# Kernel optimization log

Measured on AMD Instinct MI355X. Metric: run time of the kernel, lower is better.

Reference implementation:

```python
import jax, jax.numpy as jnp
import numpy as np

ALPHA = 0.2          # LeakyReLU negative slope
NEG_INF = -9e15      # masking value from the original module


def setup_inputs() -> dict:
    key = jax.random.key(0)
    kw, ka, k1, k2, k3 = jax.random.split(key, 5)
    B, N1, N2, F, O = 4, 2048, 2048, 256, 256
    word = jax.random.normal(kw, (B, N2, F), dtype=jnp.float32)
    # 0/1 hypergraph incidence matrix (float, as in the torch module)
    adj = jax.random.randint(ka, (B, N1, N2), 0, 2).astype(jnp.float32)
    stdv = 1.0 / np.sqrt(O)
    W1 = jax.random.uniform(k1, (F, O), jnp.float32, -stdv, stdv)
    W2 = jax.random.uniform(k2, (F, O), jnp.float32, -stdv, stdv)
    w3 = jax.random.uniform(k3, (2 * O, 1), jnp.float32, -stdv, stdv)
    return {"word": word, "adj": adj, "W1": W1, "W2": W2, "w3": w3}


def reference(word, adj, W1, W2, w3):
    # word: [B, N2, F]; adj: [B, N1, N2]; W1/W2: [F, O]; w3: [2O, 1]
    O = W1.shape[1]
    # mean-pool neighbor features per hyperedge (row-normalized adj)
    deg = jnp.sum(adj, axis=-1, keepdims=True)                 # [B, N1, 1]
    deg = jnp.where(deg > 0, deg, jnp.ones_like(deg))
    mp = jnp.matmul(adj / deg, word)                           # [B, N1, F]
    # The original builds 4D tensors h1[b,i,j,:] = adj[b,i,j]*word[b,j,:] and
    # h_mp[b,i,j,:] = adj[b,i,j]*mp[b,i,:], projects both and dots with w3.
    # Since scaling commutes with the linear maps, the scalar score is
    #   adj[b,i,j] * (word[b,j] @ W1 @ w3_a + mp[b,i] @ W2 @ w3_b)
    w3a = w3[:O, 0]                                            # pairs with w1h
    w3b = w3[O:, 0]                                            # pairs with w2h
    s1 = jnp.einsum('bnf,fo,o->bn', word, W1, w3a)             # [B, N2]
    s2 = jnp.einsum('bnf,fo,o->bn', mp, W2, w3b)               # [B, N1]
    pre = adj * (s2[:, :, None] + s1[:, None, :])              # [B, N1, N2]
    alpha = jnp.exp(jax.nn.leaky_relu(pre, ALPHA))
    attention = jnp.where(adj > 0, alpha, NEG_INF)
    attention_edge = jax.nn.softmax(attention, axis=2)         # over N2
    edge = jnp.matmul(attention_edge, word)                    # [B, N1, F]
    return edge
```

## Files before the change

kernel.cpp:

```cpp
#include <hip/hip_runtime.h>

#define B 4
#define N 2048
#define F 256
#define O 256
#define LOG2E 1.4426950408889634f
#define NEG_BIG -9000000000000000.0f

typedef _Float16 f16;
typedef f16 f16x4 __attribute__((ext_vector_type(4)));
typedef f16 f16x8 __attribute__((ext_vector_type(8)));
typedef float f32x4 __attribute__((ext_vector_type(4)));

#define WS_V1 0
#define WS_V2 256
#define WS_T1 512
#define WS_T2 (512 + B*N)
#define WT_OFF (1u << 20)
#define MK_OFF (6u << 20)

__device__ __forceinline__ float alpha_of(float pre2) {
  return __builtin_amdgcn_exp2f(fmaxf(pre2, 0.2f * pre2));
}

__global__ __launch_bounds__(256) void k_mask(const float* __restrict__ adj,
                                              unsigned* __restrict__ maskg) {
  int t = threadIdx.x;
  int wv = t >> 6, l = t & 63;
  int row = blockIdx.x * 4 + wv;
  const float* arow = adj + (size_t)row * N;
  unsigned mb = 0u;
  #pragma unroll
  for (int i = 0; i < 8; ++i) {
    float4 av = *(const float4*)(arow + i * 256 + l * 4);
    mb |= (av.x > 0.f ? (1u << (4 * i + 0)) : 0u) |
          (av.y > 0.f ? (1u << (4 * i + 1)) : 0u) |
          (av.z > 0.f ? (1u << (4 * i + 2)) : 0u) |
          (av.w > 0.f ? (1u << (4 * i + 3)) : 0u);
  }
  maskg[(size_t)row * 64 + l] = mb;
}

__global__ __launch_bounds__(256) void k_v(const float* __restrict__ W1,
                                           const float* __restrict__ W2,
                                           const float* __restrict__ w3,
                                           float* __restrict__ ws) {
  int tid = threadIdx.x;
  int lane = tid & 63;
  int f = blockIdx.x * 4 + (tid >> 6);
  float a = 0.f, b = 0.f;
  #pragma unroll
  for (int k = 0; k < 4; ++k) {
    int o = lane + 64 * k;
    a += W1[f * O + o] * w3[o];
    b += W2[f * O + o] * w3[O + o];
  }
  #pragma unroll
  for (int off = 32; off > 0; off >>= 1) {
    a += __shfl_down(a, off);
    b += __shfl_down(b, off);
  }
  if (lane == 0) {
    ws[WS_V1 + f] = a;
    ws[WS_V2 + f] = b;
  }
}

__global__ __launch_bounds__(256) void k_prep(const float* __restrict__ word,
                                              float* __restrict__ ws,
                                              f16* __restrict__ wordT) {
  __shared__ float v1s[F], v2s[F];
  __shared__ __align__(16) f16 tile[F][40];
  int t = threadIdx.x;
  int k0 = blockIdx.x * 32;
  int b = blockIdx.y;

  if (t < 64)       ((float4*)v1s)[t]      = ((const float4*)(ws + WS_V1))[t];
  else if (t < 128) ((float4*)v2s)[t - 64] = ((const float4*)(ws + WS_V2))[t - 64];
  __syncthreads();

  int r = t >> 3;
  int cg = t & 7;
  const float* wrow = word + ((size_t)(b * N + k0 + r)) * F;
  float a = 0.f, bb = 0.f;
  #pragma unroll
  for (int i = 0; i < 8; ++i) {
    int c = i * 32 + cg * 4;
    float4 w = *(const float4*)(wrow + c);
    float4 x1 = *(const float4*)(v1s + c);
    float4 x2 = *(const float4*)(v2s + c);
    a  += w.x * x1.x + w.y * x1.y + w.z * x1.z + w.w * x1.w;
    bb += w.x * x2.x + w.y * x2.y + w.z * x2.z + w.w * x2.w;
    tile[c + 0][r] = (f16)w.x;
    tile[c + 1][r] = (f16)w.y;
    tile[c + 2][r] = (f16)w.z;
    tile[c + 3][r] = (f16)w.w;
  }
  #pragma unroll
  for (int off = 4; off > 0; off >>= 1) {
    a  += __shfl_down(a, off);
    bb += __shfl_down(bb, off);
  }
  if (cg == 0) {
    ws[WS_T1 + b * N + k0 + r] = a * LOG2E;
    ws[WS_T2 + b * N + k0 + r] = bb;
  }
  __syncthreads();

  size_t base = (size_t)b * F * N;
  int kc = k0 >> 5;
  #pragma unroll
  for (int s = 0; s < 4; ++s) {
    int u = t + 256 * s;
    int ft = u >> 6, l2 = u & 63;
    f16x8 h = *(const f16x8*)&tile[ft * 16 + (l2 & 15)][(l2 >> 4) * 8];
    *(f16x8*)(wordT + base + ((size_t)(ft * 64 + kc) * 64 + l2) * 8) = h;
  }
}

__global__ __launch_bounds__(1024, 4) void k_sg(const unsigned* __restrict__ maskg,
                                                const float* __restrict__ ws,
                                                const f16* __restrict__ wordT,
                                                float* __restrict__ out) {
  extern __shared__ __align__(16) char smem[];
  float* t1S = (float*)(smem + 131072);
  float* t2S = (float*)(smem + 139264);

  const int t = threadIdx.x;
  const int wv = t >> 6, l = t & 63;
  const int bid = blockIdx.x;
  const int sbid = (bid & 7) * 32 + (bid >> 3);
  const int row0 = sbid * 32;
  const int b = row0 >> 11;

  if (t < 512) {
    *(float4*)(t1S + t * 4) = *(const float4*)(ws + WS_T1 + b * N + t * 4);
  } else {
    int u = t - 512;
    *(float4*)(t2S + u * 4) = *(const float4*)(ws + WS_T2 + b * N + u * 4);
  }
  __syncthreads();

  #pragma unroll 1
  for (int rr = 0; rr < 2; ++rr) {
    const int lrow = wv * 2 + rr;
    const unsigned mb = maskg[(size_t)(row0 + lrow) * 64 + l];

    float deg = (float)__builtin_popcount(mb);
    float dot = 0.f;
    #pragma unroll
    for (int i = 0; i < 8; ++i) {
      float4 uv = *(const float4*)(t2S + i * 256 + l * 4);
      dot += (((mb >> (4 * i + 0)) & 1u) ? uv.x : 0.f);
      dot += (((mb >> (4 * i + 1)) & 1u) ? uv.y : 0.f);
      dot += (((mb >> (4 * i + 2)) & 1u) ? uv.z : 0.f);
      dot += (((mb >> (4 * i + 3)) & 1u) ? uv.w : 0.f);
    }
    #pragma unroll
    for (int off = 32; off > 0; off >>= 1) {
      deg += __shfl_xor(deg, off);
      dot += __shfl_xor(dot, off);
    }
    float degc = deg > 0.f ? deg : 1.f;
    float s2p = (dot / degc) * LOG2E;

    float al[32];
    float m = NEG_BIG;
    #pragma unroll
    for (int i = 0; i < 8; ++i) {
      float4 pv = *(const float4*)(t1S + i * 256 + l * 4);
      const float p[4] = {pv.x, pv.y, pv.z, pv.w};
      #pragma unroll
      for (int c = 0; c < 4; ++c) {
        int j = 4 * i + c;
        al[j] = ((mb >> j) & 1u) ? alpha_of(p[c] + s2p) : NEG_BIG;
        m = fmaxf(m, al[j]);
      }
    }
    #pragma unroll
    for (int off = 32; off > 0; off >>= 1) m = fmaxf(m, __shfl_xor(m, off));

    float negmL = -m * LOG2E;
    float z = 0.f;
    #pragma unroll
    for (int j = 0; j < 32; ++j) {
      float e = __builtin_amdgcn_exp2f(fmaf(al[j], LOG2E, negmL));
      z += e;
      al[j] = e;
    }
    #pragma unroll
    for (int off = 32; off > 0; off >>= 1) z += __shfl_xor(z, off);
    float sc, wn;
    if (deg > 0.f) { sc = 1.0f / z; wn = 0.f; }
    else           { sc = 0.f;      wn = 1.0f / (float)N; }

    #pragma unroll
    for (int i = 0; i < 8; ++i) {
      f16x4 h;
      #pragma unroll
      for (int c = 0; c < 4; ++c) {
        int j = 4 * i + c;
        float w = ((mb >> j) & 1u) ? al[j] * sc : wn;
        h[c] = (f16)w;
      }
      unsigned byteoff = (unsigned)(lrow * 4096 + i * 512 + l * 8) ^ ((unsigned)(lrow & 7) << 4);
      *(f16x4*)(smem + byteoff) = h;
    }
  }
  __syncthreads();

  const int ftile = wv;
  const unsigned abase = (unsigned)((l & 15) * 4096 + (l >> 4) * 16);
  const unsigned ax = ((unsigned)(l & 7)) << 4;
  const f16* bp = wordT + (size_t)b * (F * N) + ((size_t)ftile * 64 * 64 + (size_t)l) * 8;

  f32x4 acc0 = {0.f, 0.f, 0.f, 0.f};
  f32x4 acc1 = {0.f, 0.f, 0.f, 0.f};
  #pragma unroll 8
  for (int kc = 0; kc < 64; ++kc) {
    f16x8 bf = *(const f16x8*)(bp + (size_t)kc * 512);
    f16x8 a0 = *(const f16x8*)(smem + ((abase + kc * 64) ^ ax));
    f16x8 a1 = *(const f16x8*)(smem + ((abase + 16 * 4096 + kc * 64) ^ ax));
    acc0 = __builtin_amdgcn_mfma_f32_16x16x32_f16(a0, bf, acc0, 0, 0, 0);
    acc1 = __builtin_amdgcn_mfma_f32_16x16x32_f16(a1, bf, acc1, 0, 0, 0);
  }

  const int orow = row0 + (l >> 4) * 4;
  const int c0 = ftile * 16 + (l & 15);
  #pragma unroll
  for (int reg = 0; reg < 4; ++reg) {
    out[(size_t)(orow + reg) * F + c0]      = acc0[reg];
    out[(size_t)(orow + 16 + reg) * F + c0] = acc1[reg];
  }
}

extern "C" void kernel_launch(void* const* d_in, const int* in_sizes, int n_in,
                              void* d_out, int out_size, void* d_ws, size_t ws_size,
                              hipStream_t stream) {
  const float* word = (const float*)d_in[0];
  const float* adj  = (const float*)d_in[1];
  const float* W1   = (const float*)d_in[2];
  const float* W2   = (const float*)d_in[3];
  const float* w3   = (const float*)d_in[4];
  float* out = (float*)d_out;
  float* ws  = (float*)d_ws;
  f16* wordT = (f16*)((char*)d_ws + WT_OFF);
  unsigned* maskg = (unsigned*)((char*)d_ws + MK_OFF);

  static bool s_attr = false;
  if (!s_attr) {
    hipFuncSetAttribute((const void*)k_sg, hipFuncAttributeMaxDynamicSharedMemorySize, 147456);
    s_attr = true;
  }

  k_mask<<<(B * N) / 4, 256, 0, stream>>>(adj, maskg);
  k_v<<<64, 256, 0, stream>>>(W1, W2, w3, ws);
  k_prep<<<dim3(N / 32, B), 256, 0, stream>>>(word, ws, wordT);
  k_sg<<<(B * N) / 32, 1024, 147456, stream>>>(maskg, ws, wordT, out);
}
```

Measured before the change: 130.5 us.

## Merge mask, projection-vector and prep kernels into one launch

Folds the adjacency-bitmask kernel, the W·w3 vector kernel and the word-prep kernel into a single launch. The first 2048 blocks build the mask and the remaining 256 each recompute the projection vectors redundantly before transposing word tiles. This removes two kernel launches and their serialization, and lets mask building overlap with prep work. The cost is each prep block re-reading all of W1/W2. The main kernel also hoists its mask loads ahead of the shared-memory staging barrier.

```diff
diff --git a/kernel.cpp b/kernel.cpp
--- a/kernel.cpp
+++ b/kernel.cpp
@@ -12,8 +12,6 @@
 typedef f16 f16x8 __attribute__((ext_vector_type(8)));
 typedef float f32x4 __attribute__((ext_vector_type(4)));
 
-#define WS_V1 0
-#define WS_V2 256
 #define WS_T1 512
 #define WS_T2 (512 + B*N)
 #define WT_OFF (1u << 20)
@@ -23,60 +21,60 @@
   return __builtin_amdgcn_exp2f(fmaxf(pre2, 0.2f * pre2));
 }
 
-__global__ __launch_bounds__(256) void k_mask(const float* __restrict__ adj,
-                                              unsigned* __restrict__ maskg) {
-  int t = threadIdx.x;
-  int wv = t >> 6, l = t & 63;
-  int row = blockIdx.x * 4 + wv;
-  const float* arow = adj + (size_t)row * N;
-  unsigned mb = 0u;
-  #pragma unroll
-  for (int i = 0; i < 8; ++i) {
-    float4 av = *(const float4*)(arow + i * 256 + l * 4);
-    mb |= (av.x > 0.f ? (1u << (4 * i + 0)) : 0u) |
-          (av.y > 0.f ? (1u << (4 * i + 1)) : 0u) |
-          (av.z > 0.f ? (1u << (4 * i + 2)) : 0u) |
-          (av.w > 0.f ? (1u << (4 * i + 3)) : 0u);
-  }
-  maskg[(size_t)row * 64 + l] = mb;
-}
-
-__global__ __launch_bounds__(256) void k_v(const float* __restrict__ W1,
-                                           const float* __restrict__ W2,
-                                           const float* __restrict__ w3,
-                                           float* __restrict__ ws) {
-  int tid = threadIdx.x;
-  int lane = tid & 63;
-  int f = blockIdx.x * 4 + (tid >> 6);
-  float a = 0.f, b = 0.f;
-  #pragma unroll
-  for (int k = 0; k < 4; ++k) {
-    int o = lane + 64 * k;
-    a += W1[f * O + o] * w3[o];
-    b += W2[f * O + o] * w3[O + o];
-  }
-  #pragma unroll
-  for (int off = 32; off > 0; off >>= 1) {
-    a += __shfl_down(a, off);
-    b += __shfl_down(b, off);
-  }
-  if (lane == 0) {
-    ws[WS_V1 + f] = a;
-    ws[WS_V2 + f] = b;
-  }
-}
-
-__global__ __launch_bounds__(256) void k_prep(const float* __restrict__ word,
-                                              float* __restrict__ ws,
-                                              f16* __restrict__ wordT) {
+__global__ __launch_bounds__(256) void k_mp(const float* __restrict__ adj,
+                                            const float* __restrict__ word,
+                                            const float* __restrict__ W1,
+                                            const float* __restrict__ W2,
+                                            const float* __restrict__ w3,
+                                            float* __restrict__ ws,
+                                            f16* __restrict__ wordT,
+                                            unsigned* __restrict__ maskg) {
+  __shared__ float w3s[2 * O];
   __shared__ float v1s[F], v2s[F];
   __shared__ __align__(16) f16 tile[F][40];
-  int t = threadIdx.x;
-  int k0 = blockIdx.x * 32;
-  int b = blockIdx.y;
-
-  if (t < 64)       ((float4*)v1s)[t]      = ((const float4*)(ws + WS_V1))[t];
-  else if (t < 128) ((float4*)v2s)[t - 64] = ((const float4*)(ws + WS_V2))[t - 64];
+  const int bid = blockIdx.x;
+  const int t = threadIdx.x;
+
+  if (bid < 2048) {
+    int wv = t >> 6, l = t & 63;
+    int row = bid * 4 + wv;
+    const float* arow = adj + (size_t)row * N;
+    unsigned mb = 0u;
+    #pragma unroll
+    for (int i = 0; i < 8; ++i) {
+      float4 av = *(const float4*)(arow + i * 256 + l * 4);
+      mb |= (av.x > 0.f ? (1u << (4 * i + 0)) : 0u) |
+            (av.y > 0.f ? (1u << (4 * i + 1)) : 0u) |
+            (av.z > 0.f ? (1u << (4 * i + 2)) : 0u) |
+            (av.w > 0.f ? (1u << (4 * i + 3)) : 0u);
+    }
+    maskg[(size_t)row * 64 + l] = mb;
+    return;
+  }
+
+  const int p = bid - 2048;
+  const int k0 = (p & 63) * 32;
+  const int b = p >> 6;
+
+  if (t < 128) ((float4*)w3s)[t] = ((const float4*)w3)[t];
+  __syncthreads();
+
+  {
+    float va = 0.f, vb = 0.f;
+    const float* r1 = W1 + (size_t)t * O;
+    const float* r2 = W2 + (size_t)t * O;
+    #pragma unroll 8
+    for (int i = 0; i < 64; ++i) {
+      float4 x1 = *(const float4*)(r1 + i * 4);
+      float4 x2 = *(const float4*)(r2 + i * 4);
+      va += x1.x * w3s[i * 4] + x1.y * w3s[i * 4 + 1] +
+            x1.z * w3s[i * 4 + 2] + x1.w * w3s[i * 4 + 3];
+      vb += x2.x * w3s[O + i * 4] + x2.y * w3s[O + i * 4 + 1] +
+            x2.z * w3s[O + i * 4 + 2] + x2.w * w3s[O + i * 4 + 3];
+    }
+    v1s[t] = va;
+    v2s[t] = vb;
+  }
   __syncthreads();
 
   int r = t >> 3;
@@ -133,6 +131,9 @@
   const int row0 = sbid * 32;
   const int b = row0 >> 11;
 
+  const unsigned mb0 = maskg[(size_t)(row0 + wv * 2) * 64 + l];
+  const unsigned mb1 = maskg[(size_t)(row0 + wv * 2 + 1) * 64 + l];
+
   if (t < 512) {
     *(float4*)(t1S + t * 4) = *(const float4*)(ws + WS_T1 + b * N + t * 4);
   } else {
@@ -144,7 +145,7 @@
   #pragma unroll 1
   for (int rr = 0; rr < 2; ++rr) {
     const int lrow = wv * 2 + rr;
-    const unsigned mb = maskg[(size_t)(row0 + lrow) * 64 + l];
+    const unsigned mb = rr ? mb1 : mb0;
 
     float deg = (float)__builtin_popcount(mb);
     float dot = 0.f;
@@ -253,8 +254,6 @@
     s_attr = true;
   }
 
-  k_mask<<<(B * N) / 4, 256, 0, stream>>>(adj, maskg);
-  k_v<<<64, 256, 0, stream>>>(W1, W2, w3, ws);
-  k_prep<<<dim3(N / 32, B), 256, 0, stream>>>(word, ws, wordT);
+  k_mp<<<2048 + 256, 256, 0, stream>>>(adj, word, W1, W2, w3, ws, wordT, maskg);
   k_sg<<<(B * N) / 32, 1024, 147456, stream>>>(maskg, ws, wordT, out);
 }
```

Result: slower. 153.8 us (+17.9%).
